# Kernel tuning notes

Measured on AMD Instinct MI355X. Metric: run time of the kernel, lower is better.

## Reference

```python
import jax, jax.numpy as jnp
import numpy as np

B, M, H, D, C = 512, 40, 128, 64, 128


def setup_inputs() -> dict:
    key = jax.random.key(0)
    k1, k2, k3, k4 = jax.random.split(key, 4)
    x0 = jax.random.normal(k1, (B, M, D), dtype=jnp.float32)
    xk = jax.random.normal(k2, (B, H, D), dtype=jnp.float32)
    # Conv1d(kernel_size=1) weight [C, H*M, 1] squeezed to [C, H*M]; bias [C]
    W = jax.random.normal(k3, (C, H * M), dtype=jnp.float32) * 0.02
    b = jax.random.normal(k4, (C,), dtype=jnp.float32) * 0.02
    return {"x0": x0, "xk": xk, "W": W, "b": b}


def reference(x0, xk, W, b):
    # torch: outer[b, h*M+m, d] = xk[b,h,d] * x0[b,m,d]; out = conv1d(outer)
    # conv1d with kernel_size=1 is a channel contraction:
    #   out[b,c,d] = sum_{h,m} W[c, h*M+m] * xk[b,h,d] * x0[b,m,d] + b[c]
    Bsz, Hh, Dd = xk.shape
    Mm = x0.shape[1]
    Cc = W.shape[0]
    Wr = W.reshape(Cc, Hh, Mm)  # channel index is h*M + m -> [C, H, M]
    out = jnp.einsum('bhd,bmd,chm->bcd', xk, x0, Wr) + b[None, :, None]
    return out  # [B, C, D]
```

## Files before the change

kernel.cpp:

```cpp
#include <hip/hip_runtime.h>
#include <hip/hip_bf16.h>

typedef __attribute__((ext_vector_type(8))) short short8;
typedef __attribute__((ext_vector_type(4))) float f32x4;
typedef unsigned short u16;
typedef unsigned int u32;

#define NB 512
#define NM 40
#define NH 128
#define ND 64
#define NC 128
#define KTOT 5120
#define XKP 136
#define X0P 72

__device__ __forceinline__ u16 f2bf_rne(float f) {
    u32 u = __float_as_uint(f);
    u32 r = u + 0x7FFFu + ((u >> 16) & 1u);
    return (u16)(r >> 16);
}
__device__ __forceinline__ float bf2f(short s) {
    return __uint_as_float(((u32)(u16)s) << 16);
}

__device__ __forceinline__ short8 bmul(float s, short8 xv) {
    union { short8 s8; u32 u4[4]; } r;
#pragma unroll
    for (int j = 0; j < 4; ++j) {
        float f0 = s * bf2f(xv[2 * j]);
        float f1 = s * bf2f(xv[2 * j + 1]);
        r.u4[j] = __builtin_amdgcn_perm(__float_as_uint(f1), __float_as_uint(f0),
                                        0x07060302u);
    }
    return r.s8;
}

__global__ void w3_kernel(const float* __restrict__ W, u16* __restrict__ W3) {
    __shared__ u16 kbuf[KTOT];
    const int c = blockIdx.x;
    const float* src = W + (size_t)c * KTOT;
    for (int k = threadIdx.x; k < KTOT; k += 256)
        kbuf[k] = f2bf_rne(src[k]);
    __syncthreads();
    for (int n8 = threadIdx.x; n8 < 640; n8 += 256) {
        int m = n8 % 40, hh = n8 / 40;
        union { short8 s8; u16 e[8]; } v;
#pragma unroll
        for (int j = 0; j < 8; ++j)
            v.e[j] = kbuf[hh * 320 + j * 40 + m];
        int t = n8 >> 2, q = n8 & 3;
        *(short8*)(W3 + (size_t)t * 4096 + q * 1024 + c * 8) = v.s8;
    }
}

__global__ void __launch_bounds__(256, 2) cin_main(
    const float* __restrict__ x0g, const float* __restrict__ xkg,
    const float* __restrict__ biasg, const u16* __restrict__ W3,
    float* __restrict__ out)
{
    __shared__ __align__(16) char smem[35328];
    short* xkT    = (short*)smem;
    float* x0s    = (float*)(smem + 17408);
    float* bias_s = (float*)(smem + 34816);
    float* red    = (float*)smem;

    const int tid = threadIdx.x;
    const int b = blockIdx.x;
    const int w = tid >> 6, L = tid & 63;
    const int q = L >> 4, l16 = L & 15;
    const int kh = w >> 1;
    const int rh = w & 1;

    const u16* Ap = W3 + q * 1024 + (size_t)(rh * 64 + l16) * 8;
    auto loadA = [&](int t, short8* a) {
#pragma unroll
        for (int mt = 0; mt < 4; ++mt)
            a[mt] = *(const short8*)(Ap + (size_t)t * 4096 + mt * 128);
    };

    short8 aC[4], aN[4];
    loadA(kh * 80, aC);

    {
        const float* xp = xkg + (size_t)b * (NH * ND);
        for (int i = tid; i < 2048; i += 256) {
            int h = i >> 4, d4 = (i & 15) << 2;
            float4 v = *(const float4*)(xp + h * ND + d4);
            xkT[(d4 + 0) * XKP + h] = f2bf_rne(v.x);
            xkT[(d4 + 1) * XKP + h] = f2bf_rne(v.y);
            xkT[(d4 + 2) * XKP + h] = f2bf_rne(v.z);
            xkT[(d4 + 3) * XKP + h] = f2bf_rne(v.w);
        }
        const float* x0p = x0g + (size_t)b * (NM * ND);
        for (int i = tid; i < 640; i += 256) {
            int m = i >> 4, d4 = (i & 15) << 2;
            *(f32x4*)(x0s + m * X0P + d4) = *(const f32x4*)(x0p + m * ND + d4);
        }
        if (tid < NC) bias_s[tid] = biasg[tid];
    }
    __syncthreads();

    f32x4 acc[4][4] = {};
    short8 xv[4];

    for (int tp = 0; tp < 8; ++tp) {
        const int hh = kh * 8 + tp;
#pragma unroll
        for (int n = 0; n < 4; ++n)
            xv[n] = *(const short8*)&xkT[(n * 16 + l16) * XKP + hh * 8];
#pragma unroll 2
        for (int ti = 0; ti < 10; ++ti) {
            const int tt = tp * 10 + ti;
            const int tn = (tt + 1 < 80) ? (kh * 80 + tt + 1) : kh * 80;
            loadA(tn, aN);
            const float* px0 = x0s + (4 * ti + q) * X0P + l16;
#pragma unroll
            for (int n = 0; n < 4; ++n) {
                short8 bf = bmul(px0[n * 16], xv[n]);
                acc[0][n] = __builtin_amdgcn_mfma_f32_16x16x32_bf16(aC[0], bf, acc[0][n], 0, 0, 0);
                acc[1][n] = __builtin_amdgcn_mfma_f32_16x16x32_bf16(aC[1], bf, acc[1][n], 0, 0, 0);
                acc[2][n] = __builtin_amdgcn_mfma_f32_16x16x32_bf16(aC[2], bf, acc[2][n], 0, 0, 0);
                acc[3][n] = __builtin_amdgcn_mfma_f32_16x16x32_bf16(aC[3], bf, acc[3][n], 0, 0, 0);
            }
#pragma unroll
            for (int mt = 0; mt < 4; ++mt) aC[mt] = aN[mt];
        }
    }

    __syncthreads();
    float* r0 = red + rh * 4352;
    if (kh == 1) {
#pragma unroll
        for (int mt = 0; mt < 4; ++mt)
#pragma unroll
            for (int rr = 0; rr < 4; ++rr) {
                int row = mt * 16 + q * 4 + rr;
                float* p = r0 + row * 68 + l16;
                p[0]  = acc[mt][0][rr];
                p[16] = acc[mt][1][rr];
                p[32] = acc[mt][2][rr];
                p[48] = acc[mt][3][rr];
            }
    }
    __syncthreads();
    if (kh == 0) {
        float* op = out + (size_t)b * (NC * ND);
#pragma unroll
        for (int mt = 0; mt < 4; ++mt)
#pragma unroll
            for (int rr = 0; rr < 4; ++rr) {
                int row = mt * 16 + q * 4 + rr;
                int c = rh * 64 + row;
                const float* p = r0 + row * 68 + l16;
                float bv = bias_s[c];
                op[c * ND + 0  + l16] = acc[mt][0][rr] + p[0]  + bv;
                op[c * ND + 16 + l16] = acc[mt][1][rr] + p[16] + bv;
                op[c * ND + 32 + l16] = acc[mt][2][rr] + p[32] + bv;
                op[c * ND + 48 + l16] = acc[mt][3][rr] + p[48] + bv;
            }
    }
}

extern "C" void kernel_launch(void* const* d_in, const int* in_sizes, int n_in,
                              void* d_out, int out_size, void* d_ws, size_t ws_size,
                              hipStream_t stream) {
    const float* x0 = (const float*)d_in[0];
    const float* xk = (const float*)d_in[1];
    const float* W  = (const float*)d_in[2];
    const float* bi = (const float*)d_in[3];
    float* out = (float*)d_out;

    u16* W3 = (u16*)d_ws;

    w3_kernel<<<NC, 256, 0, stream>>>(W, W3);
    cin_main<<<NB, 256, 0, stream>>>(x0, xk, bi, W3, out);
}
```

Before: 120.3 us.

## Split D columns across twice the waves and keep xk in fp32 LDS

Doubles the block to 512 threads (8 waves), with each wave covering half of the D columns, so per-wave accumulators drop from 16 to 8 tiles. xk is now stored in LDS as fp32 rather than bf16, which removes the bf16-to-fp32 unpack and uses vector multiplies before packing. LDS padding and the reduction layout change to match. More waves per block should hide MFMA and load latency better. The costs are that each wave now loads the A fragments redundantly, the larger LDS footprint may limit occupancy, and rounding changes slightly because xk*x0 is rounded once from fp32.

Result: slower. 126.5 us (+5.1%).

```diff
diff --git a/kernel.cpp b/kernel.cpp
--- a/kernel.cpp
+++ b/kernel.cpp
@@ -12,27 +12,27 @@
 #define ND 64
 #define NC 128
 #define KTOT 5120
-#define XKP 136
-#define X0P 72
+#define XKP 132
+#define X0P 68
 
 __device__ __forceinline__ u16 f2bf_rne(float f) {
     u32 u = __float_as_uint(f);
     u32 r = u + 0x7FFFu + ((u >> 16) & 1u);
     return (u16)(r >> 16);
 }
-__device__ __forceinline__ float bf2f(short s) {
-    return __uint_as_float(((u32)(u16)s) << 16);
+
+__device__ __forceinline__ u32 pack2(float f0, float f1) {
+    return __builtin_amdgcn_perm(__float_as_uint(f1), __float_as_uint(f0),
+                                 0x07060302u);
 }
 
-__device__ __forceinline__ short8 bmul(float s, short8 xv) {
+__device__ __forceinline__ short8 bmul(float s, f32x4 a, f32x4 b) {
     union { short8 s8; u32 u4[4]; } r;
-#pragma unroll
-    for (int j = 0; j < 4; ++j) {
-        float f0 = s * bf2f(xv[2 * j]);
-        float f1 = s * bf2f(xv[2 * j + 1]);
-        r.u4[j] = __builtin_amdgcn_perm(__float_as_uint(f1), __float_as_uint(f0),
-                                        0x07060302u);
-    }
+    f32x4 ma = a * s, mb = b * s;
+    r.u4[0] = pack2(ma[0], ma[1]);
+    r.u4[1] = pack2(ma[2], ma[3]);
+    r.u4[2] = pack2(mb[0], mb[1]);
+    r.u4[3] = pack2(mb[2], mb[3]);
     return r.s8;
 }
 
@@ -54,23 +54,25 @@
     }
 }
 
-__global__ void __launch_bounds__(256, 2) cin_main(
+__global__ void __launch_bounds__(512, 4) cin_main(
     const float* __restrict__ x0g, const float* __restrict__ xkg,
     const float* __restrict__ biasg, const u16* __restrict__ W3,
     float* __restrict__ out)
 {
-    __shared__ __align__(16) char smem[35328];
-    short* xkT    = (short*)smem;
-    float* x0s    = (float*)(smem + 17408);
-    float* bias_s = (float*)(smem + 34816);
+    __shared__ __align__(16) char smem[45184];
+    float* xkT    = (float*)smem;
+    float* x0s    = (float*)(smem + 33792);
+    float* bias_s = (float*)(smem + 44672);
     float* red    = (float*)smem;
 
     const int tid = threadIdx.x;
     const int b = blockIdx.x;
     const int w = tid >> 6, L = tid & 63;
     const int q = L >> 4, l16 = L & 15;
-    const int kh = w >> 1;
-    const int rh = w & 1;
+    const int kh = (w >> 2) & 1;
+    const int rh = (w >> 1) & 1;
+    const int ch = w & 1;
+    const int col0 = ch * 32 + l16;
 
     const u16* Ap = W3 + q * 1024 + (size_t)(rh * 64 + l16) * 8;
     auto loadA = [&](int t, short8* a) {
@@ -84,16 +86,16 @@
 
     {
         const float* xp = xkg + (size_t)b * (NH * ND);
-        for (int i = tid; i < 2048; i += 256) {
+        for (int i = tid; i < 2048; i += 512) {
             int h = i >> 4, d4 = (i & 15) << 2;
             float4 v = *(const float4*)(xp + h * ND + d4);
-            xkT[(d4 + 0) * XKP + h] = f2bf_rne(v.x);
-            xkT[(d4 + 1) * XKP + h] = f2bf_rne(v.y);
-            xkT[(d4 + 2) * XKP + h] = f2bf_rne(v.z);
-            xkT[(d4 + 3) * XKP + h] = f2bf_rne(v.w);
+            xkT[(d4 + 0) * XKP + h] = v.x;
+            xkT[(d4 + 1) * XKP + h] = v.y;
+            xkT[(d4 + 2) * XKP + h] = v.z;
+            xkT[(d4 + 3) * XKP + h] = v.w;
         }
         const float* x0p = x0g + (size_t)b * (NM * ND);
-        for (int i = tid; i < 640; i += 256) {
+        for (int i = tid; i < 640; i += 512) {
             int m = i >> 4, d4 = (i & 15) << 2;
             *(f32x4*)(x0s + m * X0P + d4) = *(const f32x4*)(x0p + m * ND + d4);
         }
@@ -101,27 +103,29 @@
     }
     __syncthreads();
 
-    f32x4 acc[4][4] = {};
-    short8 xv[4];
+    f32x4 acc[4][2] = {};
+    f32x4 xv[2][2];
 
     for (int tp = 0; tp < 8; ++tp) {
         const int hh = kh * 8 + tp;
 #pragma unroll
-        for (int n = 0; n < 4; ++n)
-            xv[n] = *(const short8*)&xkT[(n * 16 + l16) * XKP + hh * 8];
+        for (int n = 0; n < 2; ++n) {
+            const float* p = &xkT[(n * 16 + col0) * XKP + hh * 8];
+            xv[n][0] = *(const f32x4*)p;
+            xv[n][1] = *(const f32x4*)(p + 4);
+        }
 #pragma unroll 2
         for (int ti = 0; ti < 10; ++ti) {
             const int tt = tp * 10 + ti;
             const int tn = (tt + 1 < 80) ? (kh * 80 + tt + 1) : kh * 80;
             loadA(tn, aN);
-            const float* px0 = x0s + (4 * ti + q) * X0P + l16;
+            const float* px0 = x0s + (4 * ti + q) * X0P + col0;
+            short8 bf0 = bmul(px0[0],  xv[0][0], xv[0][1]);
+            short8 bf1 = bmul(px0[16], xv[1][0], xv[1][1]);
 #pragma unroll
-            for (int n = 0; n < 4; ++n) {
-                short8 bf = bmul(px0[n * 16], xv[n]);
-                acc[0][n] = __builtin_amdgcn_mfma_f32_16x16x32_bf16(aC[0], bf, acc[0][n], 0, 0, 0);
-                acc[1][n] = __builtin_amdgcn_mfma_f32_16x16x32_bf16(aC[1], bf, acc[1][n], 0, 0, 0);
-                acc[2][n] = __builtin_amdgcn_mfma_f32_16x16x32_bf16(aC[2], bf, acc[2][n], 0, 0, 0);
-                acc[3][n] = __builtin_amdgcn_mfma_f32_16x16x32_bf16(aC[3], bf, acc[3][n], 0, 0, 0);
+            for (int mt = 0; mt < 4; ++mt) {
+                acc[mt][0] = __builtin_amdgcn_mfma_f32_16x16x32_bf16(aC[mt], bf0, acc[mt][0], 0, 0, 0);
+                acc[mt][1] = __builtin_amdgcn_mfma_f32_16x16x32_bf16(aC[mt], bf1, acc[mt][1], 0, 0, 0);
             }
 #pragma unroll
             for (int mt = 0; mt < 4; ++mt) aC[mt] = aN[mt];
@@ -129,18 +133,15 @@
     }
 
     __syncthreads();
-    float* r0 = red + rh * 4352;
     if (kh == 1) {
 #pragma unroll
         for (int mt = 0; mt < 4; ++mt)
 #pragma unroll
             for (int rr = 0; rr < 4; ++rr) {
-                int row = mt * 16 + q * 4 + rr;
-                float* p = r0 + row * 68 + l16;
+                int row = rh * 64 + mt * 16 + q * 4 + rr;
+                float* p = red + row * 66 + col0;
                 p[0]  = acc[mt][0][rr];
                 p[16] = acc[mt][1][rr];
-                p[32] = acc[mt][2][rr];
-                p[48] = acc[mt][3][rr];
             }
     }
     __syncthreads();
@@ -150,14 +151,11 @@
         for (int mt = 0; mt < 4; ++mt)
 #pragma unroll
             for (int rr = 0; rr < 4; ++rr) {
-                int row = mt * 16 + q * 4 + rr;
-                int c = rh * 64 + row;
-                const float* p = r0 + row * 68 + l16;
-                float bv = bias_s[c];
-                op[c * ND + 0  + l16] = acc[mt][0][rr] + p[0]  + bv;
-                op[c * ND + 16 + l16] = acc[mt][1][rr] + p[16] + bv;
-                op[c * ND + 32 + l16] = acc[mt][2][rr] + p[32] + bv;
-                op[c * ND + 48 + l16] = acc[mt][3][rr] + p[48] + bv;
+                int row = rh * 64 + mt * 16 + q * 4 + rr;
+                const float* p = red + row * 66 + col0;
+                float bv = bias_s[row];
+                op[row * ND + col0]      = acc[mt][0][rr] + p[0]  + bv;
+                op[row * ND + 16 + col0] = acc[mt][1][rr] + p[16] + bv;
             }
     }
 }
@@ -174,5 +172,5 @@
     u16* W3 = (u16*)d_ws;
 
     w3_kernel<<<NC, 256, 0, stream>>>(W, W3);
-    cin_main<<<NB, 256, 0, stream>>>(x0, xk, bi, W3, out);
+    cin_main<<<NB, 512, 0, stream>>>(x0, xk, bi, W3, out);
 }
```

## Process two batches per 512-thread block with four-way K split

Applied to the files above, without the earlier changes.

Each block now handles two batch elements with 512 threads. Every loaded W3 A-fragment feeds MFMAs for both batches, which halves weight fetches per batch. The K dimension is split across four wave pairs instead of two, and partial sums are combined with a two-stage reduction through a larger LDS buffer. In exchange, each thread holds twice as many accumulators, shared memory grows to about 135 KB, and the final reduction needs extra LDS traffic and barriers.

Measured after the change: 123.5 us. +2.6%, slower.

```diff
diff --git a/kernel.cpp b/kernel.cpp
--- a/kernel.cpp
+++ b/kernel.cpp
@@ -12,8 +12,6 @@
 #define ND 64
 #define NC 128
 #define KTOT 5120
-#define XKP 136
-#define X0P 72
 
 __device__ __forceinline__ u16 f2bf_rne(float f) {
     u32 u = __float_as_uint(f);
@@ -54,23 +52,24 @@
     }
 }
 
-__global__ void __launch_bounds__(256, 2) cin_main(
+__global__ void __launch_bounds__(512, 2) cin_main(
     const float* __restrict__ x0g, const float* __restrict__ xkg,
     const float* __restrict__ biasg, const u16* __restrict__ W3,
     float* __restrict__ out)
 {
-    __shared__ __align__(16) char smem[35328];
+    __shared__ __align__(16) char smem[135680];
     short* xkT    = (short*)smem;
-    float* x0s    = (float*)(smem + 17408);
-    float* bias_s = (float*)(smem + 34816);
-    float* red    = (float*)smem;
+    float* x0s    = (float*)(smem + 34816);
+    float* bufA   = (float*)smem;
+    float* bufB   = (float*)(smem + 67584);
+    float* bias_s = (float*)(smem + 135168);
 
     const int tid = threadIdx.x;
-    const int b = blockIdx.x;
     const int w = tid >> 6, L = tid & 63;
     const int q = L >> 4, l16 = L & 15;
     const int kh = w >> 1;
     const int rh = w & 1;
+    const size_t b0 = 2 * (size_t)blockIdx.x;
 
     const u16* Ap = W3 + q * 1024 + (size_t)(rh * 64 + l16) * 8;
     auto loadA = [&](int t, short8* a) {
@@ -80,44 +79,51 @@
     };
 
     short8 aC[4], aN[4];
-    loadA(kh * 80, aC);
+    const int t0 = kh * 40;
+    loadA(t0, aC);
 
     {
-        const float* xp = xkg + (size_t)b * (NH * ND);
-        for (int i = tid; i < 2048; i += 256) {
-            int h = i >> 4, d4 = (i & 15) << 2;
-            float4 v = *(const float4*)(xp + h * ND + d4);
-            xkT[(d4 + 0) * XKP + h] = f2bf_rne(v.x);
-            xkT[(d4 + 1) * XKP + h] = f2bf_rne(v.y);
-            xkT[(d4 + 2) * XKP + h] = f2bf_rne(v.z);
-            xkT[(d4 + 3) * XKP + h] = f2bf_rne(v.w);
+        for (int i = tid; i < 4096; i += 512) {
+            int bn = i >> 11, rem = i & 2047;
+            int h = rem >> 4, d4 = (rem & 15) << 2;
+            float4 v = *(const float4*)(xkg + (b0 + bn) * (NH * ND) + h * ND + d4);
+            short* xT = xkT + bn * 8704;
+            xT[(d4 + 0) * 136 + h] = (short)f2bf_rne(v.x);
+            xT[(d4 + 1) * 136 + h] = (short)f2bf_rne(v.y);
+            xT[(d4 + 2) * 136 + h] = (short)f2bf_rne(v.z);
+            xT[(d4 + 3) * 136 + h] = (short)f2bf_rne(v.w);
         }
-        const float* x0p = x0g + (size_t)b * (NM * ND);
-        for (int i = tid; i < 640; i += 256) {
-            int m = i >> 4, d4 = (i & 15) << 2;
-            *(f32x4*)(x0s + m * X0P + d4) = *(const f32x4*)(x0p + m * ND + d4);
+        for (int i = tid; i < 1280; i += 512) {
+            int bn = i / 640, rem = i % 640;
+            int m = rem >> 4, d4 = (rem & 15) << 2;
+            *(f32x4*)(x0s + bn * 2720 + m * 68 + d4) =
+                *(const f32x4*)(x0g + (b0 + bn) * (NM * ND) + m * ND + d4);
         }
         if (tid < NC) bias_s[tid] = biasg[tid];
     }
     __syncthreads();
 
-    f32x4 acc[4][4] = {};
-    short8 xv[4];
+    f32x4 acc[4][8] = {};
+    short8 xv[8];
 
-    for (int tp = 0; tp < 8; ++tp) {
-        const int hh = kh * 8 + tp;
+    for (int tp = 0; tp < 4; ++tp) {
+        const int hh = kh * 4 + tp;
 #pragma unroll
-        for (int n = 0; n < 4; ++n)
-            xv[n] = *(const short8*)&xkT[(n * 16 + l16) * XKP + hh * 8];
+        for (int n = 0; n < 8; ++n) {
+            const short* xT = xkT + (n >> 2) * 8704;
+            xv[n] = *(const short8*)&xT[((n & 3) * 16 + l16) * 136 + hh * 8];
+        }
 #pragma unroll 2
         for (int ti = 0; ti < 10; ++ti) {
             const int tt = tp * 10 + ti;
-            const int tn = (tt + 1 < 80) ? (kh * 80 + tt + 1) : kh * 80;
+            const int tn = (tt + 1 < 40) ? (t0 + tt + 1) : t0;
             loadA(tn, aN);
-            const float* px0 = x0s + (4 * ti + q) * X0P + l16;
+            const float* p0 = x0s + (4 * ti + q) * 68 + l16;
+            const float* p1 = p0 + 2720;
 #pragma unroll
-            for (int n = 0; n < 4; ++n) {
-                short8 bf = bmul(px0[n * 16], xv[n]);
+            for (int n = 0; n < 8; ++n) {
+                float s = (n < 4) ? p0[(n & 3) * 16] : p1[(n & 3) * 16];
+                short8 bf = bmul(s, xv[n]);
                 acc[0][n] = __builtin_amdgcn_mfma_f32_16x16x32_bf16(aC[0], bf, acc[0][n], 0, 0, 0);
                 acc[1][n] = __builtin_amdgcn_mfma_f32_16x16x32_bf16(aC[1], bf, acc[1][n], 0, 0, 0);
                 acc[2][n] = __builtin_amdgcn_mfma_f32_16x16x32_bf16(aC[2], bf, acc[2][n], 0, 0, 0);
@@ -128,36 +134,51 @@
         }
     }
 
+    const int cbase = rh * 64 + q * 4;
+    auto bufp = [&](float* buf, int mt, int n) -> float* {
+        int d = (n & 3) * 16 + l16;
+        return buf + (n >> 2) * 8448 + d * 132 + cbase + mt * 16;
+    };
     __syncthreads();
-    float* r0 = red + rh * 4352;
-    if (kh == 1) {
+    if (kh & 1) {
+        float* buf = (kh == 1) ? bufA : bufB;
 #pragma unroll
         for (int mt = 0; mt < 4; ++mt)
 #pragma unroll
-            for (int rr = 0; rr < 4; ++rr) {
-                int row = mt * 16 + q * 4 + rr;
-                float* p = r0 + row * 68 + l16;
-                p[0]  = acc[mt][0][rr];
-                p[16] = acc[mt][1][rr];
-                p[32] = acc[mt][2][rr];
-                p[48] = acc[mt][3][rr];
-            }
+            for (int n = 0; n < 8; ++n)
+                *(f32x4*)bufp(buf, mt, n) = acc[mt][n];
+    }
+    __syncthreads();
+    if (!(kh & 1)) {
+        float* buf = (kh == 0) ? bufA : bufB;
+#pragma unroll
+        for (int mt = 0; mt < 4; ++mt)
+#pragma unroll
+            for (int n = 0; n < 8; ++n)
+                acc[mt][n] += *(const f32x4*)bufp(buf, mt, n);
+    }
+    __syncthreads();
+    if (kh == 2) {
+#pragma unroll
+        for (int mt = 0; mt < 4; ++mt)
+#pragma unroll
+            for (int n = 0; n < 8; ++n)
+                *(f32x4*)bufp(bufA, mt, n) = acc[mt][n];
     }
     __syncthreads();
     if (kh == 0) {
-        float* op = out + (size_t)b * (NC * ND);
 #pragma unroll
         for (int mt = 0; mt < 4; ++mt)
 #pragma unroll
-            for (int rr = 0; rr < 4; ++rr) {
-                int row = mt * 16 + q * 4 + rr;
-                int c = rh * 64 + row;
-                const float* p = r0 + row * 68 + l16;
-                float bv = bias_s[c];
-                op[c * ND + 0  + l16] = acc[mt][0][rr] + p[0]  + bv;
-                op[c * ND + 16 + l16] = acc[mt][1][rr] + p[16] + bv;
-                op[c * ND + 32 + l16] = acc[mt][2][rr] + p[32] + bv;
-                op[c * ND + 48 + l16] = acc[mt][3][rr] + p[48] + bv;
+            for (int n = 0; n < 8; ++n) {
+                acc[mt][n] += *(const f32x4*)bufp(bufA, mt, n);
+                int bn = n >> 2, d = (n & 3) * 16 + l16;
+                float* op = out + (b0 + bn) * (NC * ND);
+#pragma unroll
+                for (int rr = 0; rr < 4; ++rr) {
+                    int c = cbase + mt * 16 + rr;
+                    op[c * ND + d] = acc[mt][n][rr] + bias_s[c];
+                }
             }
     }
 }
@@ -174,5 +195,5 @@
     u16* W3 = (u16*)d_ws;
 
     w3_kernel<<<NC, 256, 0, stream>>>(W, W3);
-    cin_main<<<NB, 256, 0, stream>>>(x0, xk, bi, W3, out);
+    cin_main<<<NB / 2, 512, 0, stream>>>(x0, xk, bi, W3, out);
 }
```
